# Optimization experiments

Hardware: AMD Instinct MI355X
Metric: run time of the kernel (lower is better)

## Reference

```python
import jax, jax.numpy as jnp
import numpy as np

B, S, HIDDEN = 2, 2048, 2048
HEADS, GROUPS, KVC = 16, 4, 128
HPG = HEADS // GROUPS  # heads per group
LAYER_INDEX = 2
SOFTMAX_SCALE = KVC ** -0.5
ROPE_THETA = 10000.0


def _rope_tables(seq_len, dim, dtype=jnp.float32):
    inv_freq = 1.0 / (ROPE_THETA ** (jnp.arange(0, dim, 2, dtype=jnp.float32) / dim))
    t = jnp.arange(seq_len, dtype=jnp.float32)
    freqs = jnp.outer(t, inv_freq)  # [S, dim/2]
    return jnp.cos(freqs).astype(dtype), jnp.sin(freqs).astype(dtype)


def _apply_rope(x, cos, sin):
    # x: [b, s, h, d]; rotate-half (GPT-NeoX style)
    d2 = x.shape[-1] // 2
    x1, x2 = x[..., :d2], x[..., d2:]
    c = cos[None, :, None, :]
    s = sin[None, :, None, :]
    return jnp.concatenate([x1 * c - x2 * s, x2 * c + x1 * s], axis=-1)


def setup_inputs() -> dict:
    key = jax.random.key(0)
    k1, k2, k3, k4 = jax.random.split(key, 4)
    std = HIDDEN ** -0.5
    return {
        "x": jax.random.normal(k1, (B, S, HIDDEN), dtype=jnp.float32),
        "w_q": jax.random.normal(k2, (HIDDEN, HEADS * KVC), dtype=jnp.float32) * std,
        "w_kv": jax.random.normal(k3, (HIDDEN, 2 * GROUPS * KVC), dtype=jnp.float32) * std,
        "w_dense": jax.random.normal(k4, (HEADS * KVC, HIDDEN), dtype=jnp.float32) * std,
    }


def reference(x, w_q, w_kv, w_dense):
    b, s, _ = x.shape
    # QKV projections
    q = (x @ w_q).reshape(b, s, HEADS, KVC)                 # [b,s,H,d]
    kv = (x @ w_kv).reshape(b, s, 2, GROUPS, KVC)
    k, v = kv[:, :, 0], kv[:, :, 1]                          # [b,s,G,d]
    # Rotary embeddings on q and k
    cos, sin = _rope_tables(s, KVC, x.dtype)
    q = _apply_rope(q, cos, sin)
    k = _apply_rope(k, cos, sin)
    # GQA attention with per-layer scaling trick:
    # scores computed at scale/softmax of layer_index, cast fp32, rescaled back.
    qg = q.reshape(b, s, GROUPS, HPG, KVC)
    scores = jnp.einsum("bqghd,bkgd->bghqk", qg, k) * (SOFTMAX_SCALE / LAYER_INDEX)
    scores = scores.astype(jnp.float32) * LAYER_INDEX
    # causal mask
    causal = jnp.tril(jnp.ones((s, s), dtype=bool))
    mask_value = jnp.finfo(jnp.float32).min
    scores = jnp.where(causal[None, None, None, :, :], scores, mask_value)
    probs = jax.nn.softmax(scores, axis=-1).astype(x.dtype)  # dropout p=0 (eval)
    ctx = jnp.einsum("bghqk,bkgd->bqghd", probs, v).reshape(b, s, HEADS * KVC)
    return ctx @ w_dense
```

## Files before the change

### kernel.cpp

```cpp
#include <hip/hip_runtime.h>
#include <hip/hip_bf16.h>
#include <stdint.h>

typedef unsigned short u16;
typedef __bf16 bf16x8 __attribute__((ext_vector_type(8)));
typedef float f32x4 __attribute__((ext_vector_type(4)));

#define S_LEN 2048
#define BATCH 2
#define NHEADS 16
#define NGROUPS 4
#define DHEAD 128
#define QKV_W 3072

__device__ __forceinline__ float bf2f(u16 u) {
  union { uint32_t i; float f; } v; v.i = ((uint32_t)u) << 16; return v.f;
}
__device__ __forceinline__ u16 f2bf(float f) {
  union { float f; uint32_t i; } v; v.f = f;
  uint32_t r = v.i + 0x7FFF + ((v.i >> 16) & 1);
  return (u16)(r >> 16);
}
__device__ __forceinline__ void llds16(const void* g, void* l) {
  __builtin_amdgcn_global_load_lds(
      (const __attribute__((address_space(1))) uint32_t*)g,
      (__attribute__((address_space(3))) uint32_t*)l, 16, 0, 0);
}

__device__ __forceinline__ void store_out(u16* C, long i, float v) { C[i] = f2bf(v); }
__device__ __forceinline__ void store_out(float* C, long i, float v) { C[i] = v; }

__global__ void rope_tables_k(float* __restrict__ cosT, float* __restrict__ sinT) {
  int i = blockIdx.x * 256 + threadIdx.x;
  int s = i >> 6, j = i & 63;
  float inv = exp2f(-(float)j * 0.20762050593045983f);
  float ang = (float)s * inv;
  float sv, cv;
  sincosf(ang, &sv, &cv);
  cosT[i] = cv; sinT[i] = sv;
}

__global__ void cvt_f32_bf16(const float* __restrict__ in, u16* __restrict__ out) {
  long i = ((long)blockIdx.x * 256 + threadIdx.x) * 4;
  float4 v = *(const float4*)(in + i);
  ushort4 o;
  o.x = f2bf(v.x); o.y = f2bf(v.y); o.z = f2bf(v.z); o.w = f2bf(v.w);
  *(ushort4*)(out + i) = o;
}

__global__ void transpose_f32_bf16(const float* __restrict__ in, u16* __restrict__ out,
                                   int R, int C) {
  __shared__ u16 tile[32][33];
  int c0 = blockIdx.x * 32, r0 = blockIdx.y * 32;
  int tx = threadIdx.x, ty = threadIdx.y;
  for (int i = 0; i < 32; i += 8)
    tile[ty + i][tx] = f2bf(in[(long)(r0 + ty + i) * C + c0 + tx]);
  __syncthreads();
  for (int i = 0; i < 32; i += 8)
    out[(long)(c0 + ty + i) * R + r0 + tx] = tile[tx][ty + i];
}

template <typename OutT>
__global__ __launch_bounds__(256) void gemm_bt(
    const u16* __restrict__ A, const u16* __restrict__ Bt, OutT* __restrict__ C,
    int M, int N, int K) {
  __shared__ __align__(16) __bf16 As[128 * 32];
  __shared__ __align__(16) __bf16 Bs[128 * 32];
  const int tid = threadIdx.x;
  const int wv = tid >> 6;
  const int lane = tid & 63;
  const int quad = lane >> 4;
  const int l16 = lane & 15;
  const int bm = blockIdx.y * 128;
  const int bn = blockIdx.x * 128;

  f32x4 acc[4][4] = {};

  const int arow = wv * 32 + (lane >> 2);
  const int kseg = (lane & 3) * 8;
  const int wm = (wv >> 1) * 64, wn = (wv & 1) * 64;

  for (int k0 = 0; k0 < K; k0 += 32) {
    __syncthreads();
    const u16* ga0 = A + (long)(bm + arow) * K + k0 + kseg;
    llds16(ga0, &As[arow * 32 + kseg]);
    llds16(ga0 + (long)16 * K, &As[(arow + 16) * 32 + kseg]);
    const u16* gb0 = Bt + (long)(bn + arow) * K + k0 + kseg;
    llds16(gb0, &Bs[arow * 32 + kseg]);
    llds16(gb0 + (long)16 * K, &Bs[(arow + 16) * 32 + kseg]);
    __syncthreads();

    bf16x8 af[4], bfr[4];
#pragma unroll
    for (int mt = 0; mt < 4; ++mt)
      af[mt] = *(const bf16x8*)&As[(wm + mt * 16 + l16) * 32 + quad * 8];
#pragma unroll
    for (int nt = 0; nt < 4; ++nt)
      bfr[nt] = *(const bf16x8*)&Bs[(wn + nt * 16 + l16) * 32 + quad * 8];
#pragma unroll
    for (int mt = 0; mt < 4; ++mt)
#pragma unroll
      for (int nt = 0; nt < 4; ++nt)
        acc[mt][nt] = __builtin_amdgcn_mfma_f32_16x16x32_bf16(
            af[mt], bfr[nt], acc[mt][nt], 0, 0, 0);
  }

#pragma unroll
  for (int mt = 0; mt < 4; ++mt)
#pragma unroll
    for (int nt = 0; nt < 4; ++nt)
#pragma unroll
      for (int r = 0; r < 4; ++r) {
        int row = bm + wm + mt * 16 + quad * 4 + r;
        int col = bn + wn + nt * 16 + l16;
        store_out(C, (long)row * N + col, acc[mt][nt][r]);
      }
}

__global__ void rope_q_k(u16* __restrict__ qkv, const float* __restrict__ cosT,
                         const float* __restrict__ sinT) {
  long i = (long)blockIdx.x * 256 + threadIdx.x;
  int j = i & 63;
  long rest = i >> 6;
  int h = rest & 15;
  long bs = rest >> 4;
  int s = bs & (S_LEN - 1);
  long base = bs * QKV_W + h * DHEAD + j;
  float x1 = bf2f(qkv[base]), x2 = bf2f(qkv[base + 64]);
  float c = cosT[s * 64 + j], sn = sinT[s * 64 + j];
  qkv[base] = f2bf(x1 * c - x2 * sn);
  qkv[base + 64] = f2bf(x2 * c + x1 * sn);
}

__global__ void rope_k_k(const u16* __restrict__ qkv, u16* __restrict__ Kb,
                         const float* __restrict__ cosT, const float* __restrict__ sinT) {
  long i = (long)blockIdx.x * 256 + threadIdx.x;
  int j = i & 63;
  long rest = i >> 6;
  int g = rest & 3;
  long bs = rest >> 2;
  int s = bs & (S_LEN - 1);
  int b = (int)(bs >> 11);
  long src = bs * QKV_W + 2048 + g * 128 + j;
  float x1 = bf2f(qkv[src]), x2 = bf2f(qkv[src + 64]);
  float c = cosT[s * 64 + j], sn = sinT[s * 64 + j];
  long dst = ((long)(b * NGROUPS + g) * S_LEN + s) * DHEAD + j;
  Kb[dst] = f2bf(x1 * c - x2 * sn);
  Kb[dst + 64] = f2bf(x2 * c + x1 * sn);
}

__global__ void v_trans_k(const u16* __restrict__ qkv, u16* __restrict__ Vt) {
  __shared__ u16 tile[32][33];
  int s0 = blockIdx.x * 32, d0 = blockIdx.y * 32;
  int bg = blockIdx.z;
  int b = bg >> 2, g = bg & 3;
  int tx = threadIdx.x, ty = threadIdx.y;
  for (int i = 0; i < 32; i += 8) {
    long s = s0 + ty + i;
    tile[ty + i][tx] = qkv[((long)b * S_LEN + s) * QKV_W + 2560 + g * 128 + d0 + tx];
  }
  __syncthreads();
  for (int i = 0; i < 32; i += 8) {
    int d = d0 + ty + i;
    Vt[((long)(b * NGROUPS + g) * DHEAD + d) * S_LEN + s0 + tx] = tile[tx][ty + i];
  }
}

__global__ __launch_bounds__(256, 2) void attn_k3(
    const u16* __restrict__ Q,
    const u16* __restrict__ Kb,
    const u16* __restrict__ Vt,
    u16* __restrict__ ctx) {
  __shared__ __align__(16) __bf16 Ks[2][32 * 128];
  __shared__ __align__(16) __bf16 Vts[2][128 * 32];
  __shared__ __align__(16) __bf16 Ps[64 * 32];

  const int h = blockIdx.y, b = blockIdx.z, g = h >> 2;
  const int tid = threadIdx.x, wv = tid >> 6, lane = tid & 63;
  const int quad = lane >> 4, l16 = lane & 15;
  const float SCALE = 0.08838834764831845f;

  const long kbase = (long)(b * NGROUPS + g) * S_LEN * DHEAD;
  const long vbase = (long)(b * NGROUPS + g) * DHEAD * S_LEN;

  const int krow_off = lane >> 4;
  const int vrow_off = lane >> 2;
  const int vchunk = (lane & 3) ^ ((lane >> 2) & 3);
  const int ppos = quad ^ (l16 & 3);

  const __bf16 oneb = (__bf16)((l16 == 0) ? 1.0f : 0.0f);
  const bf16x8 bones = {oneb, oneb, oneb, oneb, oneb, oneb, oneb, oneb};

  for (int pass = 0; pass < 2; ++pass) {
    const int tile = pass == 0 ? (int)blockIdx.x : 31 - (int)blockIdx.x;
    const int q0 = tile * 64;
    const int nch = q0 / 32 + 2;

    bf16x8 aq[4];
    {
      const u16* qp = Q + (long)(b * S_LEN + q0 + wv * 16 + l16) * QKV_W + h * DHEAD + quad * 8;
#pragma unroll
      for (int ds = 0; ds < 4; ++ds)
        aq[ds] = *(const bf16x8*)(qp + ds * 32);
    }

#pragma unroll
    for (int i = 0; i < 2; ++i) {
      int r0 = wv * 8 + i * 4;
      int row = r0 + krow_off;
      int c = (lane & 15) ^ (row & 15);
      llds16(Kb + kbase + (long)row * DHEAD + c * 8, &Ks[0][r0 * 128 + lane * 8]);
    }
#pragma unroll
    for (int i = 0; i < 2; ++i) {
      int d0 = wv * 32 + i * 16;
      int row = d0 + vrow_off;
      llds16(Vt + vbase + (long)row * S_LEN + vchunk * 8, &Vts[0][d0 * 32 + lane * 8]);
    }
    __syncthreads();

    f32x4 Oacc[9] = {};

    for (int kc = 0; kc < nch; ++kc) {
      const int cur = kc & 1;
      if (kc + 1 < nch) {
        const int nxt = cur ^ 1;
#pragma unroll
        for (int i = 0; i < 2; ++i) {
          int r0 = wv * 8 + i * 4;
          int row = r0 + krow_off;
          int c = (lane & 15) ^ (row & 15);
          llds16(Kb + kbase + (long)((kc + 1) * 32 + row) * DHEAD + c * 8,
                 &Ks[nxt][r0 * 128 + lane * 8]);
        }
#pragma unroll
        for (int i = 0; i < 2; ++i) {
          int d0 = wv * 32 + i * 16;
          int row = d0 + vrow_off;
          llds16(Vt + vbase + (long)row * S_LEN + (kc + 1) * 32 + vchunk * 8,
                 &Vts[nxt][d0 * 32 + lane * 8]);
        }
      }

      f32x4 sacc[2] = {};
#pragma unroll
      for (int ds = 0; ds < 4; ++ds) {
        int pos0 = ((ds * 4 + quad) ^ l16) * 8;
        bf16x8 bk0 = *(const bf16x8*)&Ks[cur][l16 * 128 + pos0];
        bf16x8 bk1 = *(const bf16x8*)&Ks[cur][(16 + l16) * 128 + pos0];
        sacc[0] = __builtin_amdgcn_mfma_f32_16x16x32_bf16(aq[ds], bk0, sacc[0], 0, 0, 0);
        sacc[1] = __builtin_amdgcn_mfma_f32_16x16x32_bf16(aq[ds], bk1, sacc[1], 0, 0, 0);
      }

#pragma unroll
      for (int r = 0; r < 4; ++r) {
        int qrow = q0 + wv * 16 + quad * 4 + r;
        int key0 = kc * 32 + l16;
        float p0 = (key0 <= qrow) ? __expf(sacc[0][r] * SCALE) : 0.f;
        float p1 = (key0 + 16 <= qrow) ? __expf(sacc[1][r] * SCALE) : 0.f;
        int lrow = quad * 4 + r;
        int c0 = ((l16 >> 3) ^ r) * 8 + (l16 & 7);
        int c1 = (((l16 >> 3) + 2) ^ r) * 8 + (l16 & 7);
        Ps[(wv * 16 + lrow) * 32 + c0] = (__bf16)p0;
        Ps[(wv * 16 + lrow) * 32 + c1] = (__bf16)p1;
      }

      bf16x8 ap = *(const bf16x8*)&Ps[(wv * 16 + l16) * 32 + ppos * 8];
#pragma unroll
      for (int nt = 0; nt < 8; ++nt) {
        bf16x8 bv = *(const bf16x8*)&Vts[cur][(nt * 16 + l16) * 32 + ppos * 8];
        Oacc[nt] = __builtin_amdgcn_mfma_f32_16x16x32_bf16(ap, bv, Oacc[nt], 0, 0, 0);
      }
      Oacc[8] = __builtin_amdgcn_mfma_f32_16x16x32_bf16(ap, bones, Oacc[8], 0, 0, 0);

      __syncthreads();
    }

    float lsum[4];
#pragma unroll
    for (int r = 0; r < 4; ++r)
      lsum[r] = __shfl(Oacc[8][r], quad << 4, 64);

    const long obase = ((long)(b * S_LEN + q0 + wv * 16) * NHEADS + h) * DHEAD;
#pragma unroll
    for (int nt = 0; nt < 8; ++nt)
#pragma unroll
      for (int r = 0; r < 4; ++r) {
        int lrow = quad * 4 + r;
        ctx[obase + (long)lrow * NHEADS * DHEAD + nt * 16 + l16] =
            f2bf(Oacc[nt][r] / lsum[r]);
      }
  }
}

extern "C" void kernel_launch(void* const* d_in, const int* in_sizes, int n_in,
                              void* d_out, int out_size, void* d_ws, size_t ws_size,
                              hipStream_t stream) {
  const float* x   = (const float*)d_in[0];
  const float* wq  = (const float*)d_in[1];
  const float* wkv = (const float*)d_in[2];
  const float* wd  = (const float*)d_in[3];
  float* out = (float*)d_out;

  char* ws = (char*)d_ws;
  float* cosT  = (float*)(ws + 0);
  float* sinT  = (float*)(ws + 524288);
  u16* wqkvT = (u16*)(ws + 1048576);
  u16* wdT   = (u16*)(ws + 13631488);
  u16* xb    = (u16*)(ws + 22020096);
  u16* qkv   = (u16*)(ws + 38797312);
  u16* Kb    = (u16*)(ws + 63963136);
  u16* Vt    = (u16*)(ws + 68157440);
  u16* ctx   = (u16*)(ws + 72351744);

  rope_tables_k<<<512, 256, 0, stream>>>(cosT, sinT);
  cvt_f32_bf16<<<8192, 256, 0, stream>>>(x, xb);
  transpose_f32_bf16<<<dim3(64, 64), dim3(32, 8), 0, stream>>>(wq, wqkvT, 2048, 2048);
  transpose_f32_bf16<<<dim3(32, 64), dim3(32, 8), 0, stream>>>(wkv, wqkvT + (long)2048 * 2048, 2048, 1024);
  transpose_f32_bf16<<<dim3(64, 64), dim3(32, 8), 0, stream>>>(wd, wdT, 2048, 2048);

  gemm_bt<u16><<<dim3(24, 32), 256, 0, stream>>>(xb, wqkvT, qkv, 4096, 3072, 2048);

  rope_q_k<<<16384, 256, 0, stream>>>(qkv, cosT, sinT);
  rope_k_k<<<4096, 256, 0, stream>>>(qkv, Kb, cosT, sinT);
  v_trans_k<<<dim3(64, 4, 8), dim3(32, 8), 0, stream>>>(qkv, Vt);

  attn_k3<<<dim3(16, 16, 2), 256, 0, stream>>>(qkv, Kb, Vt, ctx);

  gemm_bt<float><<<dim3(16, 32), 256, 0, stream>>>(ctx, wdT, out, 4096, 2048, 2048);
}
```

Before: 330.2 us.

## Widen attention key chunk from 32 to 64 keys per iteration

Each attention loop iteration now processes 64 keys instead of 32. K, Vt and P shared buffers are doubled and the XOR swizzles are reworked for the wider tiles. This halves the number of loop iterations and block-wide barriers per query tile and gives more MFMA work between barriers. In exchange LDS use grows to about 72KB per block, which may limit occupancy under the two-blocks-per-CU launch bound, and the causal diagonal chunk does more masked work.

```diff
diff --git a/kernel.cpp b/kernel.cpp
--- a/kernel.cpp
+++ b/kernel.cpp
@@ -166,14 +166,14 @@
   }
 }
 
-__global__ __launch_bounds__(256, 2) void attn_k3(
+__global__ __launch_bounds__(256, 2) void attn_k5(
     const u16* __restrict__ Q,
     const u16* __restrict__ Kb,
     const u16* __restrict__ Vt,
     u16* __restrict__ ctx) {
-  __shared__ __align__(16) __bf16 Ks[2][32 * 128];
-  __shared__ __align__(16) __bf16 Vts[2][128 * 32];
-  __shared__ __align__(16) __bf16 Ps[64 * 32];
+  __shared__ __align__(16) __bf16 Ks[2][64 * 128];
+  __shared__ __align__(16) __bf16 Vts[2][128 * 64];
+  __shared__ __align__(16) __bf16 Ps[64 * 64];
 
   const int h = blockIdx.y, b = blockIdx.z, g = h >> 2;
   const int tid = threadIdx.x, wv = tid >> 6, lane = tid & 63;
@@ -184,9 +184,7 @@
   const long vbase = (long)(b * NGROUPS + g) * DHEAD * S_LEN;
 
   const int krow_off = lane >> 4;
-  const int vrow_off = lane >> 2;
-  const int vchunk = (lane & 3) ^ ((lane >> 2) & 3);
-  const int ppos = quad ^ (l16 & 3);
+  const int vrow_off = lane >> 3;
 
   const __bf16 oneb = (__bf16)((l16 == 0) ? 1.0f : 0.0f);
   const bf16x8 bones = {oneb, oneb, oneb, oneb, oneb, oneb, oneb, oneb};
@@ -194,7 +192,7 @@
   for (int pass = 0; pass < 2; ++pass) {
     const int tile = pass == 0 ? (int)blockIdx.x : 31 - (int)blockIdx.x;
     const int q0 = tile * 64;
-    const int nch = q0 / 32 + 2;
+    const int nch = tile + 1;
 
     bf16x8 aq[4];
     {
@@ -205,17 +203,18 @@
     }
 
 #pragma unroll
-    for (int i = 0; i < 2; ++i) {
-      int r0 = wv * 8 + i * 4;
+    for (int i = 0; i < 4; ++i) {
+      int r0 = wv * 16 + i * 4;
       int row = r0 + krow_off;
-      int c = (lane & 15) ^ (row & 15);
+      int c = l16 ^ (row & 15);
       llds16(Kb + kbase + (long)row * DHEAD + c * 8, &Ks[0][r0 * 128 + lane * 8]);
     }
 #pragma unroll
-    for (int i = 0; i < 2; ++i) {
-      int d0 = wv * 32 + i * 16;
+    for (int i = 0; i < 4; ++i) {
+      int d0 = wv * 32 + i * 8;
       int row = d0 + vrow_off;
-      llds16(Vt + vbase + (long)row * S_LEN + vchunk * 8, &Vts[0][d0 * 32 + lane * 8]);
+      int c = (lane & 7) ^ (row & 7);
+      llds16(Vt + vbase + (long)row * S_LEN + c * 8, &Vts[0][d0 * 64 + lane * 8]);
     }
     __syncthreads();
 
@@ -226,52 +225,63 @@
       if (kc + 1 < nch) {
         const int nxt = cur ^ 1;
 #pragma unroll
-        for (int i = 0; i < 2; ++i) {
-          int r0 = wv * 8 + i * 4;
+        for (int i = 0; i < 4; ++i) {
+          int r0 = wv * 16 + i * 4;
           int row = r0 + krow_off;
-          int c = (lane & 15) ^ (row & 15);
-          llds16(Kb + kbase + (long)((kc + 1) * 32 + row) * DHEAD + c * 8,
+          int c = l16 ^ (row & 15);
+          llds16(Kb + kbase + (long)((kc + 1) * 64 + row) * DHEAD + c * 8,
                  &Ks[nxt][r0 * 128 + lane * 8]);
         }
 #pragma unroll
-        for (int i = 0; i < 2; ++i) {
-          int d0 = wv * 32 + i * 16;
+        for (int i = 0; i < 4; ++i) {
+          int d0 = wv * 32 + i * 8;
           int row = d0 + vrow_off;
-          llds16(Vt + vbase + (long)row * S_LEN + (kc + 1) * 32 + vchunk * 8,
-                 &Vts[nxt][d0 * 32 + lane * 8]);
-        }
-      }
-
-      f32x4 sacc[2] = {};
+          int c = (lane & 7) ^ (row & 7);
+          llds16(Vt + vbase + (long)row * S_LEN + (kc + 1) * 64 + c * 8,
+                 &Vts[nxt][d0 * 64 + lane * 8]);
+        }
+      }
+
+      f32x4 sacc[4] = {};
 #pragma unroll
       for (int ds = 0; ds < 4; ++ds) {
         int pos0 = ((ds * 4 + quad) ^ l16) * 8;
-        bf16x8 bk0 = *(const bf16x8*)&Ks[cur][l16 * 128 + pos0];
-        bf16x8 bk1 = *(const bf16x8*)&Ks[cur][(16 + l16) * 128 + pos0];
-        sacc[0] = __builtin_amdgcn_mfma_f32_16x16x32_bf16(aq[ds], bk0, sacc[0], 0, 0, 0);
-        sacc[1] = __builtin_amdgcn_mfma_f32_16x16x32_bf16(aq[ds], bk1, sacc[1], 0, 0, 0);
-      }
-
-#pragma unroll
-      for (int r = 0; r < 4; ++r) {
-        int qrow = q0 + wv * 16 + quad * 4 + r;
-        int key0 = kc * 32 + l16;
-        float p0 = (key0 <= qrow) ? __expf(sacc[0][r] * SCALE) : 0.f;
-        float p1 = (key0 + 16 <= qrow) ? __expf(sacc[1][r] * SCALE) : 0.f;
-        int lrow = quad * 4 + r;
-        int c0 = ((l16 >> 3) ^ r) * 8 + (l16 & 7);
-        int c1 = (((l16 >> 3) + 2) ^ r) * 8 + (l16 & 7);
-        Ps[(wv * 16 + lrow) * 32 + c0] = (__bf16)p0;
-        Ps[(wv * 16 + lrow) * 32 + c1] = (__bf16)p1;
-      }
-
-      bf16x8 ap = *(const bf16x8*)&Ps[(wv * 16 + l16) * 32 + ppos * 8];
-#pragma unroll
-      for (int nt = 0; nt < 8; ++nt) {
-        bf16x8 bv = *(const bf16x8*)&Vts[cur][(nt * 16 + l16) * 32 + ppos * 8];
-        Oacc[nt] = __builtin_amdgcn_mfma_f32_16x16x32_bf16(ap, bv, Oacc[nt], 0, 0, 0);
-      }
-      Oacc[8] = __builtin_amdgcn_mfma_f32_16x16x32_bf16(ap, bones, Oacc[8], 0, 0, 0);
+#pragma unroll
+        for (int nt = 0; nt < 4; ++nt) {
+          bf16x8 bk = *(const bf16x8*)&Ks[cur][(nt * 16 + l16) * 128 + pos0];
+          sacc[nt] = __builtin_amdgcn_mfma_f32_16x16x32_bf16(aq[ds], bk, sacc[nt], 0, 0, 0);
+        }
+      }
+
+#pragma unroll
+      for (int nt = 0; nt < 4; ++nt)
+#pragma unroll
+        for (int r = 0; r < 4; ++r) {
+          int qrow = q0 + wv * 16 + quad * 4 + r;
+          int key = kc * 64 + nt * 16 + l16;
+          float p = (key <= qrow) ? __expf(sacc[nt][r] * SCALE) : 0.f;
+          int qlocal = quad * 4 + r;
+          int chunk = nt * 2 + (l16 >> 3);
+          int pos = chunk ^ (qlocal & 7);
+          Ps[(wv * 16 + qlocal) * 64 + pos * 8 + (l16 & 7)] = (__bf16)p;
+        }
+
+      bf16x8 ap[2];
+#pragma unroll
+      for (int kf = 0; kf < 2; ++kf) {
+        int pos = ((kf * 4 + quad) ^ (l16 & 7)) * 8;
+        ap[kf] = *(const bf16x8*)&Ps[(wv * 16 + l16) * 64 + pos];
+      }
+#pragma unroll
+      for (int nt = 0; nt < 8; ++nt)
+#pragma unroll
+        for (int kf = 0; kf < 2; ++kf) {
+          int pos = ((kf * 4 + quad) ^ (l16 & 7)) * 8;
+          bf16x8 bv = *(const bf16x8*)&Vts[cur][(nt * 16 + l16) * 64 + pos];
+          Oacc[nt] = __builtin_amdgcn_mfma_f32_16x16x32_bf16(ap[kf], bv, Oacc[nt], 0, 0, 0);
+        }
+      Oacc[8] = __builtin_amdgcn_mfma_f32_16x16x32_bf16(ap[0], bones, Oacc[8], 0, 0, 0);
+      Oacc[8] = __builtin_amdgcn_mfma_f32_16x16x32_bf16(ap[1], bones, Oacc[8], 0, 0, 0);
 
       __syncthreads();
     }
@@ -325,7 +335,7 @@
   rope_k_k<<<4096, 256, 0, stream>>>(qkv, Kb, cosT, sinT);
   v_trans_k<<<dim3(64, 4, 8), dim3(32, 8), 0, stream>>>(qkv, Vt);
 
-  attn_k3<<<dim3(16, 16, 2), 256, 0, stream>>>(qkv, Kb, Vt, ctx);
+  attn_k5<<<dim3(16, 16, 2), 256, 0, stream>>>(qkv, Kb, Vt, ctx);
 
   gemm_bt<float><<<dim3(16, 32), 256, 0, stream>>>(ctx, wdT, out, 4096, 2048, 2048);
 }
```

After: 318.0 us. 3.7% less time.
